# Optimization experiments

Hardware: AMD Instinct MI355X
Metric: run time of the kernel (lower is better)

The kernel has to match this reference:

```python
import jax, jax.numpy as jnp
import numpy as np

B, C, H, W = 8, 512, 64, 64
RED = 4
CR = C // RED  # 128

def setup_inputs() -> dict:
    key = jax.random.key(0)
    k1, k2, k3 = jax.random.split(key, 3)
    x = jax.random.normal(k1, (B, C, H, W), dtype=jnp.float32)
    # conv_in: 1x1 conv, no bias -> weight [3*CR, C]
    w_in = jax.random.normal(k2, (3 * CR, C), dtype=jnp.float32) * 0.02
    # conv_out: 1x1 conv, no bias -> weight [C, CR]
    w_out = jax.random.normal(k3, (C, CR), dtype=jnp.float32) * 0.02
    return {"x": x, "w_in": w_in, "w_out": w_out}

def reference(x, w_in, w_out):
    b, c, h, w = x.shape
    n = h * w
    xf = x.reshape(b, c, n)                         # flatten spatial -> [B,C,N]
    proj = jnp.einsum('oc,bcn->bon', w_in, xf)      # 1x1 conv_in -> [B,3*CR,N]
    emb_a, emb_b, g = jnp.split(proj, 3, axis=1)    # each [B,CR,N]
    # unscaled full self-attention over N spatial tokens
    weights = jnp.einsum('bcn,bcm->bnm', emb_a, emb_b)   # [B,N,N]
    weights = jax.nn.softmax(weights, axis=2)
    y = jnp.einsum('bnm,bcm->bnc', weights, g)           # [B,N,CR]
    y = jnp.einsum('oc,bnc->bon', w_out, y)              # 1x1 conv_out -> [B,C,N]
    return x + y.reshape(b, c, h, w)
```

## Files before the change

kernel.cpp:

```cpp
#include <hip/hip_runtime.h>


typedef __attribute__((ext_vector_type(8))) short short8;
typedef __attribute__((ext_vector_type(4))) float f32x4;
typedef __attribute__((ext_vector_type(16))) float f32x16;
typedef __attribute__((ext_vector_type(2))) unsigned int uint2v;

__device__ inline unsigned bfr(float f) {
  union { float f; unsigned u; } v; v.f = f;
  return v.u + 0x8000u;
}
__device__ inline unsigned short f2bf(float f) { return (unsigned short)(bfr(f) >> 16); }
__device__ inline unsigned pack2(float a, float b) {
  return __builtin_amdgcn_perm(bfr(b), bfr(a), 0x07060302u);
}
__device__ inline unsigned cvtpk(float a, float b) {
  unsigned r;
  asm("v_cvt_pk_bf16_f32 %0, %1, %2" : "=v"(r) : "v"(a), "v"(b));
  return r;
}
__device__ inline int sw(int row, int col, int stride_halves) {
  return row * stride_halves + ((((col >> 3) ^ (row & 7)) << 3) | (col & 7));
}
__device__ inline void load_lds16(const void* g, void* l) {
  __builtin_amdgcn_global_load_lds(
      (const __attribute__((address_space(1))) unsigned int*)g,
      (__attribute__((address_space(3))) unsigned int*)l, 16, 0, 0);
}

__global__ __launch_bounds__(256) void k_prep(const float* __restrict__ w_in,
                                              const float* __restrict__ w_out,
                                              unsigned short* __restrict__ wi,
                                              unsigned short* __restrict__ wo) {
  int i = blockIdx.x * 256 + threadIdx.x;
  const float* src;
  unsigned short* dst;
  int base;
  float s = 1.0f;
  if (i < 24576) {
    src = w_in;  dst = wi; base = i * 8;
    if (base < 128 * 512) s = 1.4426950408889634f;
  } else {
    src = w_out; dst = wo; base = (i - 24576) * 8;
  }
  float4 d0 = *(const float4*)&src[base];
  float4 d1 = *(const float4*)&src[base + 4];
  d0.x *= s; d0.y *= s; d0.z *= s; d0.w *= s;
  d1.x *= s; d1.y *= s; d1.z *= s; d1.w *= s;
  uint4 p;
  p.x = pack2(d0.x, d0.y); p.y = pack2(d0.z, d0.w);
  p.z = pack2(d1.x, d1.y); p.w = pack2(d1.z, d1.w);
  *(uint4*)&dst[base] = p;
}

__global__ __launch_bounds__(256, 2) void k_proj(const float* __restrict__ x,
                                                 const unsigned short* __restrict__ wi,
                                                 unsigned short* __restrict__ aq,
                                                 unsigned short* __restrict__ Kf,
                                                 unsigned short* __restrict__ Vf) {
  __shared__ unsigned short A_lds[384 * 64];
  __shared__ unsigned short B_lds[64 * 64];
  const int t = threadIdx.x;
  const int lane = t & 63;
  const int w = t >> 6;
  const int l15 = lane & 15;
  const int quad = lane >> 4;
  const int tl = blockIdx.x;
  const int n0 = tl * 64;
  const int b = blockIdx.y;
  const int ch8g = t >> 5;
  const int tp = t & 31;

  f32x4 acc[6][4];
#pragma unroll
  for (int i = 0; i < 6; i++)
#pragma unroll
    for (int j = 0; j < 4; j++) acc[i][j] = (f32x4)0.f;

  float2 d[8];
#pragma unroll
  for (int j = 0; j < 8; j++)
    d[j] = *(const float2*)&x[((size_t)(b * 512 + ch8g * 8 + j)) * 4096 + n0 + tp * 2];

  for (int k0 = 0; k0 < 512; k0 += 64) {
#pragma unroll
    for (int j = 0; j < 12; j++) {
      int row = w * 96 + j * 8 + (lane >> 3);
      int gs = (lane & 7) ^ (row & 7);
      load_lds16(&wi[(size_t)row * 512 + k0 + gs * 8],
                 (void*)&A_lds[(w * 96 + j * 8) * 64]);
    }
#pragma unroll
    for (int i = 0; i < 2; i++) {
      int r = tp * 2 + i;
      uint4 pv;
      if (i == 0) {
        pv.x = pack2(d[0].x, d[1].x); pv.y = pack2(d[2].x, d[3].x);
        pv.z = pack2(d[4].x, d[5].x); pv.w = pack2(d[6].x, d[7].x);
      } else {
        pv.x = pack2(d[0].y, d[1].y); pv.y = pack2(d[2].y, d[3].y);
        pv.z = pack2(d[4].y, d[5].y); pv.w = pack2(d[6].y, d[7].y);
      }
      *(uint4*)&B_lds[sw(r, ch8g * 8, 64)] = pv;
    }
    if (k0 + 64 < 512) {
#pragma unroll
      for (int j = 0; j < 8; j++)
        d[j] = *(const float2*)&x[((size_t)(b * 512 + k0 + 64 + ch8g * 8 + j)) * 4096 + n0 + tp * 2];
    }
    __syncthreads();
#pragma unroll
    for (int kk = 0; kk < 64; kk += 32) {
      short8 a[6];
#pragma unroll
      for (int m = 0; m < 6; m++)
        a[m] = *(const short8*)&A_lds[sw(w * 96 + m * 16 + l15, kk + quad * 8, 64)];
#pragma unroll
      for (int ns = 0; ns < 4; ns++) {
        short8 bb = *(const short8*)&B_lds[sw(ns * 16 + l15, kk + quad * 8, 64)];
#pragma unroll
        for (int m = 0; m < 6; m++)
          acc[m][ns] = __builtin_amdgcn_mfma_f32_16x16x32_bf16(a[m], bb, acc[m][ns], 0, 0, 0);
      }
    }
    __syncthreads();
  }
  const size_t tbase = ((size_t)(b * 64 + tl)) * 8192;
#pragma unroll
  for (int m = 0; m < 6; m++) {
    int o = w * 96 + m * 16 + quad * 4;
    if (o < 128) {
#pragma unroll
      for (int ns = 0; ns < 4; ns++) {
        int n = n0 + ns * 16 + l15;
        uint2 p;
        p.x = pack2(acc[m][ns][0], acc[m][ns][1]);
        p.y = pack2(acc[m][ns][2], acc[m][ns][3]);
        *(uint2*)&aq[((size_t)(b * 4096 + n)) * 128 + o] = p;
      }
    } else if (o < 256) {
      int c = o - 128;
      int ksc = c >> 4, hk = (c >> 3) & 1, e0 = c & 7;
#pragma unroll
      for (int ns = 0; ns < 4; ns++) {
        int key = ns * 16 + l15;
        int ck = (key >> 5) * 8 + ksc;
        int lane_k = hk * 32 + (key & 31);
        uint2 p;
        p.x = pack2(acc[m][ns][0], acc[m][ns][1]);
        p.y = pack2(acc[m][ns][2], acc[m][ns][3]);
        *(uint2*)&Kf[tbase + ck * 512 + lane_k * 8 + e0] = p;
      }
    } else {
      int cb = o - 256;
#pragma unroll
      for (int ns = 0; ns < 4; ns++) {
        int key = ns * 16 + l15;
        int g8 = key >> 3;
        int e = key & 7;
        size_t kb = tbase + (size_t)((g8 & 1) * 32) * 8 + e + (size_t)(g8 >> 1) * 512;
#pragma unroll
        for (int r = 0; r < 4; r++) {
          int c = cb + r;
          Vf[kb + (size_t)(c >> 5) * 4 * 512 + (size_t)(c & 31) * 8] = f2bf(acc[m][ns][r]);
        }
      }
    }
  }
}

__global__ __launch_bounds__(512, 2) void k_attn(const unsigned short* __restrict__ aq,
                                                 const unsigned short* __restrict__ Kf,
                                                 const unsigned short* __restrict__ Vf,
                                                 unsigned short* __restrict__ yt) {
  __shared__ uint4 smem4[65536 / 16];
  unsigned short* smem_h = (unsigned short*)smem4;
  float* Obuf = (float*)smem4;
  float* lsumbuf = (float*)((char*)smem4 + 33024);
  unsigned* Pbuf = (unsigned*)((char*)smem4 + 33280);

  const int t = threadIdx.x;
  const int lane = t & 63;
  const int w = t >> 6;
  const int wr = w & 1;
  const int wc = w >> 1;
  const int l31 = lane & 31;
  const int h = lane >> 5;
  const int b = blockIdx.x & 7;
  const int q0 = (blockIdx.x >> 3) * 128;

  short8 qf[8];
  {
    const unsigned short* qp = &aq[((size_t)(b * 4096 + q0 + wc * 32 + l31)) * 128 + h * 8];
#pragma unroll
    for (int ks = 0; ks < 8; ks++) qf[ks] = *(const short8*)&qp[ks * 16];
  }

  auto dma_k = [&](int tl, int buf) {
    unsigned short* Kb = smem_h + buf * 8192;
    const unsigned short* Ks = &Kf[((size_t)(b * 64 + tl)) * 8192];
#pragma unroll
    for (int j = 0; j < 2; j++) {
      int ck = w * 2 + j;
      load_lds16(&Ks[ck * 512 + lane * 8], (void*)&Kb[ck * 512]);
    }
  };
  auto dma_v = [&](int tl, int buf) {
    unsigned short* Vb = smem_h + 16384 + buf * 8192;
    const unsigned short* Vs = &Vf[((size_t)(b * 64 + tl)) * 8192];
#pragma unroll
    for (int j = 0; j < 2; j++) {
      int cv = w * 2 + j;
      load_lds16(&Vs[cv * 512 + lane * 8], (void*)&Vb[cv * 512]);
    }
  };

  f32x16 O[4];
#pragma unroll
  for (int i = 0; i < 4; i++) O[i] = (f32x16)0.f;
  float ls0 = 0.f, ls1 = 0.f, ls2 = 0.f, ls3 = 0.f;
  short8 pfP[2];

  auto computeS = [&](const unsigned short* Kc) -> f32x16 {
    f32x16 accS = (f32x16)0.f;
#pragma unroll
    for (int ks = 0; ks < 8; ks++) {
      short8 ak = *(const short8*)&Kc[(wr * 8 + ks) * 512 + lane * 8];
      accS = __builtin_amdgcn_mfma_f32_32x32x16_bf16(ak, qf[ks], accS, 0, 0, 0);
    }
    return accS;
  };
  auto computePV = [&](const unsigned short* Vc, const short8 pf[2]) {
#pragma unroll
    for (int ct = 0; ct < 4; ct++) {
#pragma unroll
      for (int f = 0; f < 2; f++) {
        short8 av = *(const short8*)&Vc[(ct * 4 + wr * 2 + f) * 512 + lane * 8];
        O[ct] = __builtin_amdgcn_mfma_f32_32x32x16_bf16(av, pf[f], O[ct], 0, 0, 0);
      }
    }
  };
  auto softmax = [&](const f32x16& accS, short8 pf[2]) {
    float ps[16];
#pragma unroll
    for (int r = 0; r < 16; r++) ps[r] = __builtin_amdgcn_exp2f(accS[r]);
    ls0 += ps[0] + ps[4];  ls1 += ps[1] + ps[5];
    ls2 += ps[2] + ps[6];  ls3 += ps[3] + ps[7];
    ls0 += ps[8] + ps[12]; ls1 += ps[9] + ps[13];
    ls2 += ps[10] + ps[14]; ls3 += ps[11] + ps[15];
    unsigned u[8];
#pragma unroll
    for (int i = 0; i < 8; i++) u[i] = cvtpk(ps[2 * i], ps[2 * i + 1]);
#pragma unroll
    for (int f = 0; f < 2; f++) {
      uint2v r02 = __builtin_amdgcn_permlane32_swap(u[4 * f + 0], u[4 * f + 2], false, false);
      uint2v r13 = __builtin_amdgcn_permlane32_swap(u[4 * f + 1], u[4 * f + 3], false, false);
      union { unsigned uu[4]; short8 s; } cv;
      cv.uu[0] = r02[0]; cv.uu[1] = r13[0]; cv.uu[2] = r02[1]; cv.uu[3] = r13[1];
      pf[f] = cv.s;
    }
  };

  dma_k(0, 0);
  dma_v(0, 0);
  __syncthreads();

  {
    dma_k(1, 1);
    __builtin_amdgcn_s_setprio(1);
    f32x16 accS = computeS(smem_h);
    __builtin_amdgcn_s_setprio(0);
    softmax(accS, pfP);
    __syncthreads();
  }

  for (int it = 1; it < 64; ++it) {
    if (it < 63) dma_k(it + 1, (it + 1) & 1);
    dma_v(it, it & 1);
    const unsigned short* Kc = smem_h + (it & 1) * 8192;
    const unsigned short* Vp = smem_h + 16384 + ((it - 1) & 1) * 8192;
    __builtin_amdgcn_s_setprio(1);
    f32x16 accS = computeS(Kc);
    computePV(Vp, pfP);
    __builtin_amdgcn_s_setprio(0);
    softmax(accS, pfP);
    __syncthreads();
  }

  {
    __builtin_amdgcn_s_setprio(1);
    computePV(smem_h + 16384 + 8192, pfP);
    __builtin_amdgcn_s_setprio(0);
  }
  __syncthreads();

  float lsum = (ls0 + ls1) + (ls2 + ls3);
  lsum += __shfl_xor(lsum, 32);
#pragma unroll
  for (int p = 0; p < 2; ++p) {
    const bool act = (wc >> 1) == p;
    const int q = (wc & 1) * 32 + l31;
    if (act && wr == 0) {
#pragma unroll
      for (int ct = 0; ct < 4; ct++)
#pragma unroll
        for (int r = 0; r < 16; r++) {
          int c = ct * 32 + (r & 3) + 8 * (r >> 2) + 4 * h;
          Obuf[q * 129 + c] = O[ct][r];
        }
      if (h == 0) lsumbuf[q] = lsum;
    }
    __syncthreads();
    if (act && wr == 1) {
      float linv = 1.f / (lsum + lsumbuf[q]);
#pragma unroll
      for (int ct = 0; ct < 4; ct++)
#pragma unroll
        for (int r = 0; r < 16; r += 2) {
          int c = ct * 32 + (r & 3) + 8 * (r >> 2) + 4 * h;
          float v0 = (Obuf[q * 129 + c] + O[ct][r]) * linv;
          float v1 = (Obuf[q * 129 + c + 1] + O[ct][r + 1]) * linv;
          Pbuf[q * 65 + (c >> 1)] = pack2(v0, v1);
        }
    }
    __syncthreads();
    {
      int qq = t >> 3, seg = t & 7;
      unsigned* yrow = (unsigned*)&yt[((size_t)(b * 4096 + q0 + p * 64 + qq)) * 128];
#pragma unroll
      for (int i = 0; i < 2; i++) {
        int base = qq * 65 + seg * 8 + i * 4;
        uint4 v;
        v.x = Pbuf[base + 0];
        v.y = Pbuf[base + 1];
        v.z = Pbuf[base + 2];
        v.w = Pbuf[base + 3];
        *(uint4*)&yrow[seg * 8 + i * 4] = v;
      }
    }
  }
}

__global__ __launch_bounds__(256) void k_out(const float* __restrict__ x,
                                             const unsigned short* __restrict__ wo,
                                             const unsigned short* __restrict__ yt,
                                             float* __restrict__ out) {
  __shared__ unsigned short A_lds[128 * 128];
  __shared__ unsigned short B_lds[64 * 128];
  const int t = threadIdx.x;
  const int lane = t & 63;
  const int w = t >> 6;
  const int l15 = lane & 15;
  const int quad = lane >> 4;
  const int id = blockIdx.x;
  const int b = id & 7;
  const int rest = id >> 3;
  const int o0 = (rest & 3) * 128;
  const int n0 = (rest >> 2) * 64;

#pragma unroll
  for (int j = 0; j < 8; j++) {
    int row = w * 32 + j * 4 + (lane >> 4);
    int gs = (lane & 15) ^ (row & 7);
    load_lds16(&wo[(size_t)(o0 + row) * 128 + gs * 8],
               (void*)&A_lds[(w * 32 + j * 4) * 128]);
  }
#pragma unroll
  for (int j = 0; j < 4; j++) {
    int row = w * 16 + j * 4 + (lane >> 4);
    int gs = (lane & 15) ^ (row & 7);
    load_lds16(&yt[((size_t)(b * 4096 + n0 + row)) * 128 + gs * 8],
               (void*)&B_lds[(w * 16 + j * 4) * 128]);
  }
  __syncthreads();

  f32x4 acc[2][4];
#pragma unroll
  for (int i = 0; i < 2; i++)
#pragma unroll
    for (int j = 0; j < 4; j++) acc[i][j] = (f32x4)0.f;
#pragma unroll
  for (int ks = 0; ks < 4; ks++) {
    short8 a0 = *(const short8*)&A_lds[sw(w * 32 + l15, ks * 32 + quad * 8, 128)];
    short8 a1 = *(const short8*)&A_lds[sw(w * 32 + 16 + l15, ks * 32 + quad * 8, 128)];
#pragma unroll
    for (int ns = 0; ns < 4; ns++) {
      short8 bb = *(const short8*)&B_lds[sw(ns * 16 + l15, ks * 32 + quad * 8, 128)];
      acc[0][ns] = __builtin_amdgcn_mfma_f32_16x16x32_bf16(a0, bb, acc[0][ns], 0, 0, 0);
      acc[1][ns] = __builtin_amdgcn_mfma_f32_16x16x32_bf16(a1, bb, acc[1][ns], 0, 0, 0);
    }
  }
#pragma unroll
  for (int ms = 0; ms < 2; ms++) {
    int o = o0 + w * 32 + ms * 16 + quad * 4;
#pragma unroll
    for (int ns = 0; ns < 4; ns++) {
      int n = n0 + ns * 16 + l15;
#pragma unroll
      for (int r = 0; r < 4; r++) {
        size_t off = ((size_t)(b * 512 + o + r)) * 4096 + n;
        out[off] = x[off] + acc[ms][ns][r];
      }
    }
  }
}

extern "C" void kernel_launch(void* const* d_in, const int* in_sizes, int n_in,
                              void* d_out, int out_size, void* d_ws, size_t ws_size,
                              hipStream_t stream) {
  const float* x = (const float*)d_in[0];
  const float* w_in = (const float*)d_in[1];
  const float* w_out = (const float*)d_in[2];
  float* out = (float*)d_out;

  unsigned short* aq = (unsigned short*)d_ws;
  unsigned short* Kf = aq + (size_t)8 * 4096 * 128;
  unsigned short* Vf = Kf + (size_t)8 * 64 * 8192;
  unsigned short* yt = Vf + (size_t)8 * 64 * 8192;
  unsigned short* wi = yt + (size_t)8 * 4096 * 128;
  unsigned short* wo = wi + (size_t)384 * 512;

  k_prep<<<128, 256, 0, stream>>>(w_in, w_out, wi, wo);
  k_proj<<<dim3(64, 8), 256, 0, stream>>>(x, wi, aq, Kf, Vf);
  k_attn<<<dim3(256), 512, 0, stream>>>(aq, Kf, Vf, yt);
  k_out<<<2048, 256, 0, stream>>>(x, wo, yt, out);
}
```

Measured before the change: 211.4 us.

## Fuse output projection and residual add into attention epilogue

Removes the separate k_out kernel and the bf16 yt intermediate. The attention kernel now normalizes the whole 128-query tile at once into LDS, then streams pre-swizzled w_out fragments through LDS and does the 1x1 output conv plus the residual add in place. The w_out weights are written in MFMA-fragment order by k_prep. The kernel uses about 99KB of dynamic LDS and launch bounds drop to one block per CU. That can hurt latency hiding during the attention main loop, which now runs 256 blocks at lower occupancy.

```diff
diff --git a/kernel.cpp b/kernel.cpp
--- a/kernel.cpp
+++ b/kernel.cpp
@@ -31,26 +31,31 @@
 __global__ __launch_bounds__(256) void k_prep(const float* __restrict__ w_in,
                                               const float* __restrict__ w_out,
                                               unsigned short* __restrict__ wi,
-                                              unsigned short* __restrict__ wo) {
+                                              unsigned short* __restrict__ wf) {
   int i = blockIdx.x * 256 + threadIdx.x;
-  const float* src;
-  unsigned short* dst;
-  int base;
-  float s = 1.0f;
   if (i < 24576) {
-    src = w_in;  dst = wi; base = i * 8;
-    if (base < 128 * 512) s = 1.4426950408889634f;
+    int base = i * 8;
+    float s = (base < 128 * 512) ? 1.4426950408889634f : 1.0f;
+    float4 d0 = *(const float4*)&w_in[base];
+    float4 d1 = *(const float4*)&w_in[base + 4];
+    d0.x *= s; d0.y *= s; d0.z *= s; d0.w *= s;
+    d1.x *= s; d1.y *= s; d1.z *= s; d1.w *= s;
+    uint4 p;
+    p.x = pack2(d0.x, d0.y); p.y = pack2(d0.z, d0.w);
+    p.z = pack2(d1.x, d1.y); p.w = pack2(d1.z, d1.w);
+    *(uint4*)&wi[base] = p;
   } else {
-    src = w_out; dst = wo; base = (i - 24576) * 8;
-  }
-  float4 d0 = *(const float4*)&src[base];
-  float4 d1 = *(const float4*)&src[base + 4];
-  d0.x *= s; d0.y *= s; d0.z *= s; d0.w *= s;
-  d1.x *= s; d1.y *= s; d1.z *= s; d1.w *= s;
-  uint4 p;
-  p.x = pack2(d0.x, d0.y); p.y = pack2(d0.z, d0.w);
-  p.z = pack2(d1.x, d1.y); p.w = pack2(d1.z, d1.w);
-  *(uint4*)&dst[base] = p;
+    int base = (i - 24576) * 8;
+    int o = base >> 7, c0 = base & 127;
+    float4 d0 = *(const float4*)&w_out[base];
+    float4 d1 = *(const float4*)&w_out[base + 4];
+    uint4 p;
+    p.x = pack2(d0.x, d0.y); p.y = pack2(d0.z, d0.w);
+    p.z = pack2(d1.x, d1.y); p.w = pack2(d1.z, d1.w);
+    int chunk = (o >> 4) * 4 + (c0 >> 5);
+    int lane = (o & 15) + ((c0 >> 3) & 3) * 16;
+    *(uint4*)&wf[chunk * 512 + lane * 8] = p;
+  }
 }
 
 __global__ __launch_bounds__(256, 2) void k_proj(const float* __restrict__ x,
@@ -169,15 +174,16 @@
   }
 }
 
-__global__ __launch_bounds__(512, 2) void k_attn(const unsigned short* __restrict__ aq,
+__global__ __launch_bounds__(512, 1) void k_attn(const unsigned short* __restrict__ aq,
                                                  const unsigned short* __restrict__ Kf,
                                                  const unsigned short* __restrict__ Vf,
-                                                 unsigned short* __restrict__ yt) {
-  __shared__ uint4 smem4[65536 / 16];
-  unsigned short* smem_h = (unsigned short*)smem4;
-  float* Obuf = (float*)smem4;
-  float* lsumbuf = (float*)((char*)smem4 + 33024);
-  unsigned* Pbuf = (unsigned*)((char*)smem4 + 33280);
+                                                 const unsigned short* __restrict__ wf,
+                                                 const float* __restrict__ x,
+                                                 float* __restrict__ out) {
+  extern __shared__ unsigned short smem_h[];
+  float* Obuf = (float*)smem_h;
+  float* lsumbuf = (float*)((char*)smem_h + 66048);
+  unsigned* Pbuf = (unsigned*)((char*)smem_h + 66560);
 
   const int t = threadIdx.x;
   const int lane = t & 63;
@@ -186,6 +192,8 @@
   const int wc = w >> 1;
   const int l31 = lane & 31;
   const int h = lane >> 5;
+  const int l15 = lane & 15;
+  const int quad = lane >> 4;
   const int b = blockIdx.x & 7;
   const int q0 = (blockIdx.x >> 3) * 128;
 
@@ -296,112 +304,75 @@
 
   float lsum = (ls0 + ls1) + (ls2 + ls3);
   lsum += __shfl_xor(lsum, 32);
-#pragma unroll
-  for (int p = 0; p < 2; ++p) {
-    const bool act = (wc >> 1) == p;
-    const int q = (wc & 1) * 32 + l31;
-    if (act && wr == 0) {
-#pragma unroll
-      for (int ct = 0; ct < 4; ct++)
-#pragma unroll
-        for (int r = 0; r < 16; r++) {
-          int c = ct * 32 + (r & 3) + 8 * (r >> 2) + 4 * h;
-          Obuf[q * 129 + c] = O[ct][r];
+  const int q = wc * 32 + l31;
+  if (wr == 0) {
+#pragma unroll
+    for (int ct = 0; ct < 4; ct++)
+#pragma unroll
+      for (int r = 0; r < 16; r++) {
+        int c = ct * 32 + (r & 3) + 8 * (r >> 2) + 4 * h;
+        Obuf[q * 129 + c] = O[ct][r];
+      }
+    if (h == 0) lsumbuf[q] = lsum;
+  }
+  __syncthreads();
+  if (wr == 1) {
+    float linv = 1.f / (lsum + lsumbuf[q]);
+#pragma unroll
+    for (int ct = 0; ct < 4; ct++)
+#pragma unroll
+      for (int r = 0; r < 16; r += 2) {
+        int c = ct * 32 + (r & 3) + 8 * (r >> 2) + 4 * h;
+        float v0 = (Obuf[q * 129 + c] + O[ct][r]) * linv;
+        float v1 = (Obuf[q * 129 + c + 1] + O[ct][r + 1]) * linv;
+        Pbuf[q * 68 + (c >> 1)] = pack2(v0, v1);
+      }
+  }
+  __syncthreads();
+
+  unsigned short* Wp = smem_h;
+  for (int p = 0; p < 4; ++p) {
+#pragma unroll
+    for (int j = 0; j < 4; j++) {
+      int cl = w * 4 + j;
+      load_lds16(&wf[(p * 32 + cl) * 512 + lane * 8], (void*)&Wp[cl * 512]);
+    }
+    __syncthreads();
+
+    f32x4 acc[2][4];
+#pragma unroll
+    for (int i = 0; i < 2; i++)
+#pragma unroll
+      for (int j = 0; j < 4; j++) acc[i][j] = (f32x4)0.f;
+#pragma unroll
+    for (int ks = 0; ks < 4; ks++) {
+      short8 a[2];
+#pragma unroll
+      for (int i = 0; i < 2; i++)
+        a[i] = *(const short8*)&Wp[(((w & 3) * 2 + i) * 4 + ks) * 512 + lane * 8];
+#pragma unroll
+      for (int nt = 0; nt < 4; nt++) {
+        int token = ((w >> 2) * 4 + nt) * 16 + l15;
+        short8 bb = *(const short8*)&Pbuf[token * 68 + ks * 16 + quad * 4];
+#pragma unroll
+        for (int i = 0; i < 2; i++)
+          acc[i][nt] = __builtin_amdgcn_mfma_f32_16x16x32_bf16(a[i], bb, acc[i][nt], 0, 0, 0);
+      }
+    }
+#pragma unroll
+    for (int i = 0; i < 2; i++) {
+      int o = p * 128 + ((w & 3) * 2 + i) * 16 + quad * 4;
+#pragma unroll
+      for (int nt = 0; nt < 4; nt++) {
+        int n = q0 + ((w >> 2) * 4 + nt) * 16 + l15;
+#pragma unroll
+        for (int r = 0; r < 4; r++) {
+          size_t off = ((size_t)(b * 512 + o + r)) * 4096 + n;
+          out[off] = x[off] + acc[i][nt][r];
         }
-      if (h == 0) lsumbuf[q] = lsum;
-    }
-    __syncthreads();
-    if (act && wr == 1) {
-      float linv = 1.f / (lsum + lsumbuf[q]);
-#pragma unroll
-      for (int ct = 0; ct < 4; ct++)
-#pragma unroll
-        for (int r = 0; r < 16; r += 2) {
-          int c = ct * 32 + (r & 3) + 8 * (r >> 2) + 4 * h;
-          float v0 = (Obuf[q * 129 + c] + O[ct][r]) * linv;
-          float v1 = (Obuf[q * 129 + c + 1] + O[ct][r + 1]) * linv;
-          Pbuf[q * 65 + (c >> 1)] = pack2(v0, v1);
-        }
-    }
-    __syncthreads();
-    {
-      int qq = t >> 3, seg = t & 7;
-      unsigned* yrow = (unsigned*)&yt[((size_t)(b * 4096 + q0 + p * 64 + qq)) * 128];
-#pragma unroll
-      for (int i = 0; i < 2; i++) {
-        int base = qq * 65 + seg * 8 + i * 4;
-        uint4 v;
-        v.x = Pbuf[base + 0];
-        v.y = Pbuf[base + 1];
-        v.z = Pbuf[base + 2];
-        v.w = Pbuf[base + 3];
-        *(uint4*)&yrow[seg * 8 + i * 4] = v;
-      }
-    }
-  }
-}
-
-__global__ __launch_bounds__(256) void k_out(const float* __restrict__ x,
-                                             const unsigned short* __restrict__ wo,
-                                             const unsigned short* __restrict__ yt,
-                                             float* __restrict__ out) {
-  __shared__ unsigned short A_lds[128 * 128];
-  __shared__ unsigned short B_lds[64 * 128];
-  const int t = threadIdx.x;
-  const int lane = t & 63;
-  const int w = t >> 6;
-  const int l15 = lane & 15;
-  const int quad = lane >> 4;
-  const int id = blockIdx.x;
-  const int b = id & 7;
-  const int rest = id >> 3;
-  const int o0 = (rest & 3) * 128;
-  const int n0 = (rest >> 2) * 64;
-
-#pragma unroll
-  for (int j = 0; j < 8; j++) {
-    int row = w * 32 + j * 4 + (lane >> 4);
-    int gs = (lane & 15) ^ (row & 7);
-    load_lds16(&wo[(size_t)(o0 + row) * 128 + gs * 8],
-               (void*)&A_lds[(w * 32 + j * 4) * 128]);
-  }
-#pragma unroll
-  for (int j = 0; j < 4; j++) {
-    int row = w * 16 + j * 4 + (lane >> 4);
-    int gs = (lane & 15) ^ (row & 7);
-    load_lds16(&yt[((size_t)(b * 4096 + n0 + row)) * 128 + gs * 8],
-               (void*)&B_lds[(w * 16 + j * 4) * 128]);
-  }
-  __syncthreads();
-
-  f32x4 acc[2][4];
-#pragma unroll
-  for (int i = 0; i < 2; i++)
-#pragma unroll
-    for (int j = 0; j < 4; j++) acc[i][j] = (f32x4)0.f;
-#pragma unroll
-  for (int ks = 0; ks < 4; ks++) {
-    short8 a0 = *(const short8*)&A_lds[sw(w * 32 + l15, ks * 32 + quad * 8, 128)];
-    short8 a1 = *(const short8*)&A_lds[sw(w * 32 + 16 + l15, ks * 32 + quad * 8, 128)];
-#pragma unroll
-    for (int ns = 0; ns < 4; ns++) {
-      short8 bb = *(const short8*)&B_lds[sw(ns * 16 + l15, ks * 32 + quad * 8, 128)];
-      acc[0][ns] = __builtin_amdgcn_mfma_f32_16x16x32_bf16(a0, bb, acc[0][ns], 0, 0, 0);
-      acc[1][ns] = __builtin_amdgcn_mfma_f32_16x16x32_bf16(a1, bb, acc[1][ns], 0, 0, 0);
-    }
-  }
-#pragma unroll
-  for (int ms = 0; ms < 2; ms++) {
-    int o = o0 + w * 32 + ms * 16 + quad * 4;
-#pragma unroll
-    for (int ns = 0; ns < 4; ns++) {
-      int n = n0 + ns * 16 + l15;
-#pragma unroll
-      for (int r = 0; r < 4; r++) {
-        size_t off = ((size_t)(b * 512 + o + r)) * 4096 + n;
-        out[off] = x[off] + acc[ms][ns][r];
-      }
-    }
+      }
+    }
+    __syncthreads();
   }
 }
 
@@ -416,12 +387,17 @@
   unsigned short* aq = (unsigned short*)d_ws;
   unsigned short* Kf = aq + (size_t)8 * 4096 * 128;
   unsigned short* Vf = Kf + (size_t)8 * 64 * 8192;
-  unsigned short* yt = Vf + (size_t)8 * 64 * 8192;
-  unsigned short* wi = yt + (size_t)8 * 4096 * 128;
-  unsigned short* wo = wi + (size_t)384 * 512;
-
-  k_prep<<<128, 256, 0, stream>>>(w_in, w_out, wi, wo);
+  unsigned short* wf = Vf + (size_t)8 * 64 * 8192;
+  unsigned short* wi = wf + (size_t)128 * 512;
+
+  static bool attr_set = false;
+  if (!attr_set) {
+    hipFuncSetAttribute((const void*)k_attn,
+                        hipFuncAttributeMaxDynamicSharedMemorySize, 101376);
+    attr_set = true;
+  }
+
+  k_prep<<<128, 256, 0, stream>>>(w_in, w_out, wi, wf);
   k_proj<<<dim3(64, 8), 256, 0, stream>>>(x, wi, aq, Kf, Vf);
-  k_attn<<<dim3(256), 512, 0, stream>>>(aq, Kf, Vf, yt);
-  k_out<<<2048, 256, 0, stream>>>(x, wo, yt, out);
-}
+  k_attn<<<dim3(256), 512, 101376, stream>>>(aq, Kf, Vf, wf, x, out);
+}
```

Result: no change. 210.2 us (-0.5%).
